# Kernel optimization log

Hardware: AMD Instinct MI355X
Metric: run time of the kernel (lower is better)

Reference implementation:

```python
import jax, jax.numpy as jnp
import numpy as np

D_MODEL = 512
NUM_HEADS = 8
D_K = D_MODEL // NUM_HEADS
EPS = 1e-8


def setup_inputs() -> dict:
    key = jax.random.key(0)
    ks = jax.random.split(key, 11)
    B, N = 2, 2048
    s = 1.0 / np.sqrt(D_MODEL)
    return {
        "query": jax.random.normal(ks[0], (B, N, D_MODEL), jnp.float32),
        "key": jax.random.normal(ks[1], (B, N, D_MODEL), jnp.float32),
        "value": jax.random.normal(ks[2], (B, N, D_MODEL), jnp.float32),
        "Wq": jax.random.uniform(ks[3], (D_MODEL, D_MODEL), jnp.float32, -s, s),
        "bq": jax.random.uniform(ks[4], (D_MODEL,), jnp.float32, -s, s),
        "Wk": jax.random.uniform(ks[5], (D_MODEL, D_MODEL), jnp.float32, -s, s),
        "bk": jax.random.uniform(ks[6], (D_MODEL,), jnp.float32, -s, s),
        "Wv": jax.random.uniform(ks[7], (D_MODEL, D_MODEL), jnp.float32, -s, s),
        "bv": jax.random.uniform(ks[8], (D_MODEL,), jnp.float32, -s, s),
        "Wo": jax.random.uniform(ks[9], (D_MODEL, D_MODEL), jnp.float32, -s, s),
        "bo": jax.random.uniform(ks[10], (D_MODEL,), jnp.float32, -s, s),
    }


def _heads(x, W, b, B):
    # torch Linear: x @ W.T + b ; then [B,N,H,dk] -> [B,H,N,dk]
    y = x @ W.T + b
    return y.reshape(B, -1, NUM_HEADS, D_K).transpose(0, 2, 1, 3)


def reference(query, key, value, Wq, bq, Wk, bk, Wv, bv, Wo, bo):
    B = query.shape[0]
    Q = _heads(query, Wq, bq, B)
    K = _heads(key, Wk, bk, B)
    V = _heads(value, Wv, bv, B)
    # elu(x) + 1 feature map
    Q = jax.nn.elu(Q) + 1.0
    K = jax.nn.elu(K) + 1.0
    # normalize Q over feature dim, K over sequence dim
    Qn = Q / (Q.sum(axis=-1, keepdims=True) + EPS)
    Kn = K / (K.sum(axis=-2, keepdims=True) + EPS)
    # explicit NxN context matrix (as in the original code)
    attention_weights = jnp.einsum("bhnd,bhmd->bhnm", Qn, Kn)  # [B,H,N,N]
    out = jnp.einsum("bhnm,bhmd->bhnd", attention_weights, V)   # [B,H,N,dk]
    out = out.transpose(0, 2, 1, 3).reshape(B, -1, D_MODEL)
    out = out @ Wo.T + bo
    return (out, attention_weights)
```

## Files before the change

### kernel.cpp

```cpp
#include <hip/hip_runtime.h>

#define B2    2
#define NSEQ  2048
#define DM    512
#define NH    8
#define DK    64
#define MROWS 4096
#define BH    (B2*NH)
#define BHSTR (NSEQ*DK)
#define EPSF  1e-8f
#define OUT0  (MROWS*DM)

typedef __attribute__((ext_vector_type(8))) short short8;
typedef __attribute__((ext_vector_type(4))) float f32x4;

union S8 { short8 v; short s[8]; };
union F4 { f32x4 v; float f[4]; };

__device__ float          g_Qp[MROWS*DM];
__device__ float          g_Kn[MROWS*DM];
__device__ float          g_Vh[MROWS*DM];
__device__ float          g_OH[MROWS*DM];
__device__ unsigned short g_Qbf[MROWS*DM];
__device__ unsigned short g_Kbf[MROWS*DM];
__device__ float          g_qinv[BH*NSEQ];
__device__ float          g_ksum[BH*DK];
__device__ float          g_KV[BH*DK*DK];

__device__ inline unsigned short f2bf(float x) {
    union { float f; unsigned u; } v; v.f = x;
    unsigned r = v.u + 0x7fffu + ((v.u >> 16) & 1u);
    return (unsigned short)(r >> 16);
}
__device__ inline float bf2f(unsigned short h) {
    union { unsigned u; float f; } v; v.u = ((unsigned)h) << 16; return v.f;
}
__device__ inline f32x4 mfma_bf16(short8 a, short8 b, f32x4 c) {
    return __builtin_amdgcn_mfma_f32_16x16x32_bf16(a, b, c, 0, 0, 0);
}

__global__ void zero_small() {
    int i = blockIdx.x * 256 + threadIdx.x;
    if (i < BH*DK*DK) g_KV[i] = 0.f;
    if (i < BH*DK)    g_ksum[i] = 0.f;
}

__global__ __launch_bounds__(256) void gemm_split(const float* __restrict__ A,
                                                  const float* __restrict__ W,
                                                  const float* __restrict__ bias,
                                                  float* __restrict__ dout, int mode) {
    __shared__ short Ah[128*56], Al[128*56], Bh_s[64*56], Bl_s[64*56];

    const float* Ap = (mode == 3) ? (const float*)g_OH : A;

    int t = threadIdx.x;
    int m0 = blockIdx.x * 128, n0 = blockIdx.y * 64;
    int lane = t & 63, w = t >> 6;
    int l15 = lane & 15, quad = lane >> 4;

    f32x4 acc[2][4];
    f32x4 z4 = {0.f, 0.f, 0.f, 0.f};
#pragma unroll
    for (int i = 0; i < 2; i++)
#pragma unroll
        for (int j = 0; j < 4; j++) acc[i][j] = z4;

    int ar = t >> 1, ac = (t & 1) * 16;
    int br = t >> 2, bc = (t & 3) * 8;

    for (int k0 = 0; k0 < 512; k0 += 32) {
        {
            const float* ag = Ap + (size_t)(m0 + ar) * 512 + k0 + ac;
            float xv[16];
            *(f32x4*)&xv[0]  = *(const f32x4*)(ag + 0);
            *(f32x4*)&xv[4]  = *(const f32x4*)(ag + 4);
            *(f32x4*)&xv[8]  = *(const f32x4*)(ag + 8);
            *(f32x4*)&xv[12] = *(const f32x4*)(ag + 12);
            S8 h0, h1, l0, l1;
#pragma unroll
            for (int i = 0; i < 8; i++) {
                float x = xv[i];
                unsigned short hb = f2bf(x);
                h0.s[i] = (short)hb;
                l0.s[i] = (short)f2bf(x - bf2f(hb));
            }
#pragma unroll
            for (int i = 0; i < 8; i++) {
                float x = xv[8 + i];
                unsigned short hb = f2bf(x);
                h1.s[i] = (short)hb;
                l1.s[i] = (short)f2bf(x - bf2f(hb));
            }
            *(short8*)&Ah[ar*56 + ac]     = h0.v;
            *(short8*)&Ah[ar*56 + ac + 8] = h1.v;
            *(short8*)&Al[ar*56 + ac]     = l0.v;
            *(short8*)&Al[ar*56 + ac + 8] = l1.v;
        }
        {
            const float* wg = W + (size_t)(n0 + br) * 512 + k0 + bc;
            float xv[8];
            *(f32x4*)&xv[0] = *(const f32x4*)(wg + 0);
            *(f32x4*)&xv[4] = *(const f32x4*)(wg + 4);
            S8 h0, l0;
#pragma unroll
            for (int i = 0; i < 8; i++) {
                float x = xv[i];
                unsigned short hb = f2bf(x);
                h0.s[i] = (short)hb;
                l0.s[i] = (short)f2bf(x - bf2f(hb));
            }
            *(short8*)&Bh_s[br*56 + bc] = h0.v;
            *(short8*)&Bl_s[br*56 + bc] = l0.v;
        }
        __syncthreads();

        int koff = quad * 8;
        short8 a_h[2], a_l[2], b_h[4], b_l[4];
#pragma unroll
        for (int i = 0; i < 2; i++) {
            int rr = (w*32 + i*16 + l15) * 56 + koff;
            a_h[i] = *(const short8*)&Ah[rr];
            a_l[i] = *(const short8*)&Al[rr];
        }
#pragma unroll
        for (int j = 0; j < 4; j++) {
            int rr = (j*16 + l15) * 56 + koff;
            b_h[j] = *(const short8*)&Bh_s[rr];
            b_l[j] = *(const short8*)&Bl_s[rr];
        }
#pragma unroll
        for (int i = 0; i < 2; i++)
#pragma unroll
            for (int j = 0; j < 4; j++) {
                acc[i][j] = mfma_bf16(a_h[i], b_h[j], acc[i][j]);
                acc[i][j] = mfma_bf16(a_h[i], b_l[j], acc[i][j]);
                acc[i][j] = mfma_bf16(a_l[i], b_h[j], acc[i][j]);
            }
        __syncthreads();
    }

#pragma unroll
    for (int j = 0; j < 4; j++) {
        int col = n0 + j*16 + l15;
        float bs = bias[col];
#pragma unroll
        for (int i = 0; i < 2; i++) {
            F4 v; v.v = acc[i][j];
#pragma unroll
            for (int r = 0; r < 4; r++) {
                int row = m0 + w*32 + i*16 + quad*4 + r;
                float val = v.f[r] + bs;
                if (mode == 3) {
                    dout[(size_t)row * 512 + col] = val;
                } else {
                    int bb = row >> 11, nn = row & 2047;
                    int hh = col >> 6,  dd = col & 63;
                    int dst = (bb*8 + hh) * BHSTR + nn*64 + dd;
                    if (mode == 2) {
                        g_Vh[dst] = val;
                    } else {
                        float e = (val > 0.f) ? (val + 1.f) : expf(val);
                        if (mode == 0) { g_Qp[dst] = e; g_Qbf[dst] = f2bf(e); }
                        else           { g_Kn[dst] = e; }
                    }
                }
            }
        }
    }
}

__global__ void qsum_kernel() {
    int t = threadIdx.x, w = t >> 6, lane = t & 63;
    int row = blockIdx.x * 4 + w;
    float v = g_Qp[(size_t)row * 64 + lane];
#pragma unroll
    for (int off = 32; off; off >>= 1) v += __shfl_down(v, off, 64);
    if (lane == 0) g_qinv[row] = 1.f / (v + EPSF);
}

__global__ void ksum_kernel() {
    int t = threadIdx.x;
    int bh = blockIdx.x >> 3, part = blockIdx.x & 7;
    int d = t & 63, sub = t >> 6;
    float s = 0.f;
    size_t base = (size_t)bh * BHSTR + (size_t)(part * 256) * 64 + d;
    for (int i = 0; i < 64; i++) s += g_Kn[base + (size_t)(sub + i*4) * 64];
    __shared__ float red[256];
    red[t] = s;
    __syncthreads();
    if (t < 64) {
        float tot = red[t] + red[t+64] + red[t+128] + red[t+192];
        atomicAdd(&g_ksum[bh*64 + d], tot);
    }
}

__global__ void knorm_kernel() {
    int gid = blockIdx.x * 256 + threadIdx.x;
    int i0 = gid * 4;
    int bh = i0 >> 17, d0 = i0 & 63;
    F4 v; v.v = *(const f32x4*)&g_Kn[i0];
    F4 o;
    unsigned short b[4];
#pragma unroll
    for (int j = 0; j < 4; j++) {
        float r = v.f[j] / (g_ksum[bh*64 + d0 + j] + EPSF);
        o.f[j] = r;
        b[j] = f2bf(r);
    }
    *(f32x4*)&g_Kn[i0] = o.v;
    unsigned long long packed = (unsigned long long)b[0] | ((unsigned long long)b[1] << 16)
                              | ((unsigned long long)b[2] << 32) | ((unsigned long long)b[3] << 48);
    *(unsigned long long*)&g_Kbf[i0] = packed;
}

__global__ __launch_bounds__(256) void attn_kernel(float* __restrict__ dout) {
    __shared__ short Qs[128*72], Ks[128*72];
    int bh = blockIdx.z;
    int m0 = blockIdx.x * 128, n0 = blockIdx.y * 128;
    int t = threadIdx.x, lane = t & 63, w = t >> 6;
    int l15 = lane & 15, quad = lane >> 4;

    int r = t >> 1, c0 = (t & 1) * 32;
    const short* qg = (const short*)g_Qbf + (size_t)bh * BHSTR + (size_t)(m0 + r) * 64 + c0;
    const short* kg = (const short*)g_Kbf + (size_t)bh * BHSTR + (size_t)(n0 + r) * 64 + c0;
#pragma unroll
    for (int i = 0; i < 4; i++) {
        *(short8*)&Qs[r*72 + c0 + 8*i] = *(const short8*)(qg + 8*i);
        *(short8*)&Ks[r*72 + c0 + 8*i] = *(const short8*)(kg + 8*i);
    }
    __syncthreads();

    int wm = (w >> 1) * 64, wn = (w & 1) * 64;
    f32x4 acc[4][4];
    f32x4 z4 = {0.f, 0.f, 0.f, 0.f};
#pragma unroll
    for (int i = 0; i < 4; i++)
#pragma unroll
        for (int j = 0; j < 4; j++) acc[i][j] = z4;

#pragma unroll
    for (int kk = 0; kk < 64; kk += 32) {
        short8 qa[4], kb[4];
#pragma unroll
        for (int i = 0; i < 4; i++) qa[i] = *(const short8*)&Qs[(wm + i*16 + l15)*72 + kk + quad*8];
#pragma unroll
        for (int j = 0; j < 4; j++) kb[j] = *(const short8*)&Ks[(wn + j*16 + l15)*72 + kk + quad*8];
#pragma unroll
        for (int i = 0; i < 4; i++)
#pragma unroll
            for (int j = 0; j < 4; j++) acc[i][j] = mfma_bf16(qa[i], kb[j], acc[i][j]);
    }

    float* outp = dout + OUT0 + (size_t)bh * NSEQ * NSEQ;
#pragma unroll
    for (int i = 0; i < 4; i++) {
#pragma unroll
        for (int r2 = 0; r2 < 4; r2++) {
            int row = m0 + wm + i*16 + quad*4 + r2;
            float qiv = g_qinv[bh*NSEQ + row];
#pragma unroll
            for (int j = 0; j < 4; j++) {
                int col = n0 + wn + j*16 + l15;
                F4 v; v.v = acc[i][j];
                outp[(size_t)row * NSEQ + col] = v.f[r2] * qiv;
            }
        }
    }
}

__global__ __launch_bounds__(256) void kv_kernel() {
    __shared__ float Ks2[64*64], Vs[64*64];
    int bh = blockIdx.x >> 4, part = blockIdx.x & 15;
    int t = threadIdx.x, d = t & 63, e0 = (t >> 6) * 16;
    float accv[16];
#pragma unroll
    for (int i = 0; i < 16; i++) accv[i] = 0.f;
    int sr = t >> 2, sc = (t & 3) * 16;
    for (int c = 0; c < 2; c++) {
        int nbase = part * 128 + c * 64;
        const float* kgp = g_Kn + (size_t)bh * BHSTR + (size_t)(nbase + sr) * 64 + sc;
        const float* vgp = g_Vh + (size_t)bh * BHSTR + (size_t)(nbase + sr) * 64 + sc;
#pragma unroll
        for (int i = 0; i < 4; i++) {
            *(f32x4*)&Ks2[sr*64 + sc + 4*i] = *(const f32x4*)(kgp + 4*i);
            *(f32x4*)&Vs[sr*64 + sc + 4*i]  = *(const f32x4*)(vgp + 4*i);
        }
        __syncthreads();
#pragma unroll 4
        for (int m = 0; m < 64; m++) {
            float v = Vs[m*64 + d];
            const f32x4* kr = (const f32x4*)&Ks2[m*64 + e0];
            F4 k0, k1, k2, k3;
            k0.v = kr[0]; k1.v = kr[1]; k2.v = kr[2]; k3.v = kr[3];
#pragma unroll
            for (int i = 0; i < 4; i++) accv[i]      += k0.f[i] * v;
#pragma unroll
            for (int i = 0; i < 4; i++) accv[4 + i]  += k1.f[i] * v;
#pragma unroll
            for (int i = 0; i < 4; i++) accv[8 + i]  += k2.f[i] * v;
#pragma unroll
            for (int i = 0; i < 4; i++) accv[12 + i] += k3.f[i] * v;
        }
        __syncthreads();
    }
#pragma unroll
    for (int i = 0; i < 16; i++)
        atomicAdd(&g_KV[bh*4096 + (e0 + i)*64 + d], accv[i]);
}

__global__ __launch_bounds__(256) void oh_kernel() {
    __shared__ float Qs2[128*64];
    __shared__ float KVs[64*64];
    int bh = blockIdx.y, r0 = blockIdx.x * 128;
    int t = threadIdx.x, d = t & 63, w = t >> 6;
    {
        int r = t >> 2, c = (t & 3) * 16;
        const float* s = g_KV + bh*4096 + r*64 + c;
#pragma unroll
        for (int i = 0; i < 4; i++) *(f32x4*)&KVs[r*64 + c + 4*i] = *(const f32x4*)(s + 4*i);
    }
    {
        int r = t >> 1, c = (t & 1) * 32;
        const float* s = g_Qp + (size_t)bh * BHSTR + (size_t)(r0 + r) * 64 + c;
#pragma unroll
        for (int i = 0; i < 8; i++) *(f32x4*)&Qs2[r*64 + c + 4*i] = *(const f32x4*)(s + 4*i);
    }
    __syncthreads();
    float kvc[64];
#pragma unroll
    for (int e = 0; e < 64; e++) kvc[e] = KVs[e*64 + d];
    int b = bh >> 3, h = bh & 7;
    for (int rr = 0; rr < 32; rr++) {
        int row = w * 32 + rr;
        const f32x4* qr = (const f32x4*)&Qs2[row*64];
        float a = 0.f;
#pragma unroll
        for (int e4 = 0; e4 < 16; e4++) {
            F4 q; q.v = qr[e4];
            a += q.f[0]*kvc[4*e4] + q.f[1]*kvc[4*e4+1] + q.f[2]*kvc[4*e4+2] + q.f[3]*kvc[4*e4+3];
        }
        int grow = r0 + row;
        float val = a * g_qinv[bh*NSEQ + grow];
        g_OH[((size_t)b*NSEQ + grow)*512 + h*64 + d] = val;
    }
}

extern "C" void kernel_launch(void* const* d_in, const int* in_sizes, int n_in,
                              void* d_out, int out_size, void* d_ws, size_t ws_size,
                              hipStream_t stream) {
    const float* q  = (const float*)d_in[0];
    const float* k  = (const float*)d_in[1];
    const float* v  = (const float*)d_in[2];
    const float* Wq = (const float*)d_in[3];
    const float* bq = (const float*)d_in[4];
    const float* Wk = (const float*)d_in[5];
    const float* bk = (const float*)d_in[6];
    const float* Wv = (const float*)d_in[7];
    const float* bv = (const float*)d_in[8];
    const float* Wo = (const float*)d_in[9];
    const float* bo = (const float*)d_in[10];
    float* out = (float*)d_out;

    zero_small<<<256, 256, 0, stream>>>();

    dim3 gproj(32, 8);
    gemm_split<<<gproj, 256, 0, stream>>>(q, Wq, bq, out, 0);
    gemm_split<<<gproj, 256, 0, stream>>>(k, Wk, bk, out, 1);
    gemm_split<<<gproj, 256, 0, stream>>>(v, Wv, bv, out, 2);

    qsum_kernel<<<8192, 256, 0, stream>>>();
    ksum_kernel<<<128, 256, 0, stream>>>();
    knorm_kernel<<<2048, 256, 0, stream>>>();

    attn_kernel<<<dim3(16, 16, BH), 256, 0, stream>>>(out);

    kv_kernel<<<256, 256, 0, stream>>>();
    oh_kernel<<<dim3(16, BH), 256, 0, stream>>>();

    gemm_split<<<gproj, 256, 0, stream>>>(nullptr, Wo, bo, out, 3);
}
```

Before: 471.5 us.

## Pre-split inputs to bf16, fuse normalization into GEMM epilogues, use direct-to-LDS loads

A new prep kernel converts inputs and weights to bf16 hi/lo pairs once, replacing the per-tile conversion inside the GEMMs. The GEMMs now load tiles with global_load_lds into XOR-swizzled shared memory. The K-sum, Q row sums and K normalization move into the GEMM epilogues, which removes the separate qsum, ksum and knorm kernels. V and the Wo input use a single bf16 term instead of the split, and intermediates are stored as bf16. This cuts conversion work, launches and memory traffic, but V and the output projection lose precision and K is rounded to bf16 before normalization.

Result: faster. 405.1 us (-14.1%).

```diff
diff --git a/kernel.cpp b/kernel.cpp
--- a/kernel.cpp
+++ b/kernel.cpp
@@ -1,62 +1,115 @@
 #include <hip/hip_runtime.h>
-
-#define B2    2
+#include <math.h>
+
 #define NSEQ  2048
 #define DM    512
 #define NH    8
 #define DK    64
 #define MROWS 4096
-#define BH    (B2*NH)
+#define BH    16
 #define BHSTR (NSEQ*DK)
+#define SLAB  (BH*BHSTR)
 #define EPSF  1e-8f
 #define OUT0  (MROWS*DM)
 
 typedef __attribute__((ext_vector_type(8))) short short8;
 typedef __attribute__((ext_vector_type(4))) float f32x4;
-
 union S8 { short8 v; short s[8]; };
 union F4 { f32x4 v; float f[4]; };
 
-__device__ float          g_Qp[MROWS*DM];
-__device__ float          g_Kn[MROWS*DM];
-__device__ float          g_Vh[MROWS*DM];
-__device__ float          g_OH[MROWS*DM];
-__device__ unsigned short g_Qbf[MROWS*DM];
-__device__ unsigned short g_Kbf[MROWS*DM];
+__device__ short g_qh[MROWS*DM], g_ql[MROWS*DM];
+__device__ short g_kh[MROWS*DM], g_kl[MROWS*DM];
+__device__ short g_vh[MROWS*DM];
+__device__ short g_wqh[DM*DM], g_wql[DM*DM];
+__device__ short g_wkh[DM*DM], g_wkl[DM*DM];
+__device__ short g_wvh[DM*DM], g_woh[DM*DM];
+__device__ unsigned short g_Qbf[SLAB];
+__device__ unsigned short g_Kbf[SLAB];
+__device__ float          g_Vf[SLAB];
+__device__ short          g_OHbf[MROWS*DM];
 __device__ float          g_qinv[BH*NSEQ];
 __device__ float          g_ksum[BH*DK];
 __device__ float          g_KV[BH*DK*DK];
 
-__device__ inline unsigned short f2bf(float x) {
+__device__ __forceinline__ unsigned short f2bf(float x) {
     union { float f; unsigned u; } v; v.f = x;
     unsigned r = v.u + 0x7fffu + ((v.u >> 16) & 1u);
     return (unsigned short)(r >> 16);
 }
-__device__ inline float bf2f(unsigned short h) {
+__device__ __forceinline__ float bf2f(unsigned short h) {
     union { unsigned u; float f; } v; v.u = ((unsigned)h) << 16; return v.f;
 }
-__device__ inline f32x4 mfma_bf16(short8 a, short8 b, f32x4 c) {
+__device__ __forceinline__ f32x4 mfma_bf16(short8 a, short8 b, f32x4 c) {
     return __builtin_amdgcn_mfma_f32_16x16x32_bf16(a, b, c, 0, 0, 0);
 }
-
-__global__ void zero_small() {
-    int i = blockIdx.x * 256 + threadIdx.x;
-    if (i < BH*DK*DK) g_KV[i] = 0.f;
-    if (i < BH*DK)    g_ksum[i] = 0.f;
-}
-
-__global__ __launch_bounds__(256) void gemm_split(const float* __restrict__ A,
-                                                  const float* __restrict__ W,
-                                                  const float* __restrict__ bias,
-                                                  float* __restrict__ dout, int mode) {
-    __shared__ short Ah[128*56], Al[128*56], Bh_s[64*56], Bl_s[64*56];
-
-    const float* Ap = (mode == 3) ? (const float*)g_OH : A;
-
-    int t = threadIdx.x;
+__device__ __forceinline__ float elu1(float x) {
+    return (x > 0.f) ? (x + 1.f) : __expf(x);
+}
+__device__ __forceinline__ void gl_lds16(const void* gsrc, void* ldst) {
+    __builtin_amdgcn_global_load_lds(
+        (__attribute__((address_space(1))) void*)(unsigned long long)(gsrc),
+        (__attribute__((address_space(3))) void*)(unsigned)(unsigned long long)(ldst),
+        16, 0, 0);
+}
+
+__global__ __launch_bounds__(256) void prep_kernel(const float* __restrict__ q, const float* __restrict__ k,
+                                                   const float* __restrict__ v, const float* __restrict__ wq,
+                                                   const float* __restrict__ wk, const float* __restrict__ wv,
+                                                   const float* __restrict__ wo) {
+    int b = blockIdx.x, t = threadIdx.x;
+    if (b < 33) {
+        int z = b * 2048 + t * 8;
+#pragma unroll
+        for (int i = 0; i < 8; i++) {
+            int zz = z + i;
+            if (zz < 65536) g_KV[zz] = 0.f;
+            else if (zz < 66560) g_ksum[zz - 65536] = 0.f;
+        }
+    }
+    const float* src; short* hi; short* lo; int off; int split;
+    if (b < 1024)      { src = q;  hi = g_qh;  lo = g_ql;  off = b * 2048;          split = 1; }
+    else if (b < 2048) { src = k;  hi = g_kh;  lo = g_kl;  off = (b-1024) * 2048;   split = 1; }
+    else if (b < 3072) { src = v;  hi = g_vh;  lo = g_vh;  off = (b-2048) * 2048;   split = 0; }
+    else if (b < 3200) { src = wq; hi = g_wqh; lo = g_wql; off = (b-3072) * 2048;   split = 1; }
+    else if (b < 3328) { src = wk; hi = g_wkh; lo = g_wkl; off = (b-3200) * 2048;   split = 1; }
+    else if (b < 3456) { src = wv; hi = g_wvh; lo = g_wvh; off = (b-3328) * 2048;   split = 0; }
+    else               { src = wo; hi = g_woh; lo = g_woh; off = (b-3456) * 2048;   split = 0; }
+    int idx = off + t * 8;
+    F4 a0, a1; a0.v = *(const f32x4*)(src + idx); a1.v = *(const f32x4*)(src + idx + 4);
+    S8 h, l;
+#pragma unroll
+    for (int i = 0; i < 4; i++) {
+        unsigned short hb = f2bf(a0.f[i]); h.s[i] = (short)hb;
+        l.s[i] = (short)f2bf(a0.f[i] - bf2f(hb));
+    }
+#pragma unroll
+    for (int i = 0; i < 4; i++) {
+        unsigned short hb = f2bf(a1.f[i]); h.s[4+i] = (short)hb;
+        l.s[4+i] = (short)f2bf(a1.f[i] - bf2f(hb));
+    }
+    *(short8*)(hi + idx) = h.v;
+    if (split) *(short8*)(lo + idx) = l.v;
+}
+
+template<int SPLIT>
+__global__ __launch_bounds__(256) void gemm_bf16(const float* __restrict__ bias,
+                                                 float* __restrict__ dout, int mode) {
+    __shared__ short sAh[128*64];
+    __shared__ short sBh[64*64];
+    __shared__ short sAl[SPLIT ? 128*64 : 8];
+    __shared__ short sBl[SPLIT ? 64*64 : 8];
+
+    const short *Ahi, *Alo = nullptr, *Bhi, *Blo = nullptr;
+    if (mode == 0)      { Ahi = g_qh;   Alo = g_ql;  Bhi = g_wqh; Blo = g_wql; }
+    else if (mode == 1) { Ahi = g_kh;   Alo = g_kl;  Bhi = g_wkh; Blo = g_wkl; }
+    else if (mode == 2) { Ahi = g_vh;   Bhi = g_wvh; }
+    else                { Ahi = g_OHbf; Bhi = g_woh; }
+
+    int t = threadIdx.x, lane = t & 63, w = t >> 6;
+    int l15 = lane & 15, quad = lane >> 4;
     int m0 = blockIdx.x * 128, n0 = blockIdx.y * 64;
-    int lane = t & 63, w = t >> 6;
-    int l15 = lane & 15, quad = lane >> 4;
+    int r_in = lane >> 3, gq = lane & 7;
+    int scol = (gq ^ r_in) << 3;
 
     f32x4 acc[2][4];
     f32x4 z4 = {0.f, 0.f, 0.f, 0.f};
@@ -65,168 +118,162 @@
 #pragma unroll
         for (int j = 0; j < 4; j++) acc[i][j] = z4;
 
-    int ar = t >> 1, ac = (t & 1) * 16;
-    int br = t >> 2, bc = (t & 3) * 8;
-
-    for (int k0 = 0; k0 < 512; k0 += 32) {
-        {
-            const float* ag = Ap + (size_t)(m0 + ar) * 512 + k0 + ac;
-            float xv[16];
-            *(f32x4*)&xv[0]  = *(const f32x4*)(ag + 0);
-            *(f32x4*)&xv[4]  = *(const f32x4*)(ag + 4);
-            *(f32x4*)&xv[8]  = *(const f32x4*)(ag + 8);
-            *(f32x4*)&xv[12] = *(const f32x4*)(ag + 12);
-            S8 h0, h1, l0, l1;
-#pragma unroll
-            for (int i = 0; i < 8; i++) {
-                float x = xv[i];
-                unsigned short hb = f2bf(x);
-                h0.s[i] = (short)hb;
-                l0.s[i] = (short)f2bf(x - bf2f(hb));
-            }
-#pragma unroll
-            for (int i = 0; i < 8; i++) {
-                float x = xv[8 + i];
-                unsigned short hb = f2bf(x);
-                h1.s[i] = (short)hb;
-                l1.s[i] = (short)f2bf(x - bf2f(hb));
-            }
-            *(short8*)&Ah[ar*56 + ac]     = h0.v;
-            *(short8*)&Ah[ar*56 + ac + 8] = h1.v;
-            *(short8*)&Al[ar*56 + ac]     = l0.v;
-            *(short8*)&Al[ar*56 + ac + 8] = l1.v;
-        }
-        {
-            const float* wg = W + (size_t)(n0 + br) * 512 + k0 + bc;
-            float xv[8];
-            *(f32x4*)&xv[0] = *(const f32x4*)(wg + 0);
-            *(f32x4*)&xv[4] = *(const f32x4*)(wg + 4);
-            S8 h0, l0;
-#pragma unroll
-            for (int i = 0; i < 8; i++) {
-                float x = xv[i];
-                unsigned short hb = f2bf(x);
-                h0.s[i] = (short)hb;
-                l0.s[i] = (short)f2bf(x - bf2f(hb));
-            }
-            *(short8*)&Bh_s[br*56 + bc] = h0.v;
-            *(short8*)&Bl_s[br*56 + bc] = l0.v;
+    for (int k0 = 0; k0 < 512; k0 += 64) {
+#pragma unroll
+        for (int ii = 0; ii < 4; ii++) {
+            int i = w * 4 + ii;
+            size_t so = (size_t)(m0 + i*8 + r_in) * 512 + k0 + scol;
+            gl_lds16(Ahi + so, &sAh[i * 512]);
+            if (SPLIT) gl_lds16(Alo + so, &sAl[i * 512]);
+        }
+#pragma unroll
+        for (int ii = 0; ii < 2; ii++) {
+            int i = w * 2 + ii;
+            size_t so = (size_t)(n0 + i*8 + r_in) * 512 + k0 + scol;
+            gl_lds16(Bhi + so, &sBh[i * 512]);
+            if (SPLIT) gl_lds16(Blo + so, &sBl[i * 512]);
         }
         __syncthreads();
 
-        int koff = quad * 8;
-        short8 a_h[2], a_l[2], b_h[4], b_l[4];
-#pragma unroll
-        for (int i = 0; i < 2; i++) {
-            int rr = (w*32 + i*16 + l15) * 56 + koff;
-            a_h[i] = *(const short8*)&Ah[rr];
-            a_l[i] = *(const short8*)&Al[rr];
-        }
-#pragma unroll
-        for (int j = 0; j < 4; j++) {
-            int rr = (j*16 + l15) * 56 + koff;
-            b_h[j] = *(const short8*)&Bh_s[rr];
-            b_l[j] = *(const short8*)&Bl_s[rr];
-        }
-#pragma unroll
-        for (int i = 0; i < 2; i++)
+#pragma unroll
+        for (int ks = 0; ks < 2; ks++) {
+            int kg = ks * 4 + quad;
+            int sw = (kg ^ (l15 & 7)) << 3;
+            short8 ah[2], al[2], bh[4], bl[4];
+#pragma unroll
+            for (int i = 0; i < 2; i++) {
+                int ad = (w*32 + i*16 + l15) * 64 + sw;
+                ah[i] = *(const short8*)&sAh[ad];
+                if (SPLIT) al[i] = *(const short8*)&sAl[ad];
+            }
 #pragma unroll
             for (int j = 0; j < 4; j++) {
-                acc[i][j] = mfma_bf16(a_h[i], b_h[j], acc[i][j]);
-                acc[i][j] = mfma_bf16(a_h[i], b_l[j], acc[i][j]);
-                acc[i][j] = mfma_bf16(a_l[i], b_h[j], acc[i][j]);
-            }
-        __syncthreads();
-    }
-
-#pragma unroll
-    for (int j = 0; j < 4; j++) {
-        int col = n0 + j*16 + l15;
-        float bs = bias[col];
-#pragma unroll
-        for (int i = 0; i < 2; i++) {
-            F4 v; v.v = acc[i][j];
-#pragma unroll
-            for (int r = 0; r < 4; r++) {
-                int row = m0 + w*32 + i*16 + quad*4 + r;
-                float val = v.f[r] + bs;
-                if (mode == 3) {
-                    dout[(size_t)row * 512 + col] = val;
-                } else {
-                    int bb = row >> 11, nn = row & 2047;
-                    int hh = col >> 6,  dd = col & 63;
-                    int dst = (bb*8 + hh) * BHSTR + nn*64 + dd;
-                    if (mode == 2) {
-                        g_Vh[dst] = val;
-                    } else {
-                        float e = (val > 0.f) ? (val + 1.f) : expf(val);
-                        if (mode == 0) { g_Qp[dst] = e; g_Qbf[dst] = f2bf(e); }
-                        else           { g_Kn[dst] = e; }
+                int ad = (j*16 + l15) * 64 + sw;
+                bh[j] = *(const short8*)&sBh[ad];
+                if (SPLIT) bl[j] = *(const short8*)&sBl[ad];
+            }
+#pragma unroll
+            for (int i = 0; i < 2; i++)
+#pragma unroll
+                for (int j = 0; j < 4; j++) {
+                    acc[i][j] = mfma_bf16(ah[i], bh[j], acc[i][j]);
+                    if (SPLIT) {
+                        acc[i][j] = mfma_bf16(ah[i], bl[j], acc[i][j]);
+                        acc[i][j] = mfma_bf16(al[i], bh[j], acc[i][j]);
                     }
                 }
-            }
-        }
-    }
-}
-
-__global__ void qsum_kernel() {
-    int t = threadIdx.x, w = t >> 6, lane = t & 63;
-    int row = blockIdx.x * 4 + w;
-    float v = g_Qp[(size_t)row * 64 + lane];
-#pragma unroll
-    for (int off = 32; off; off >>= 1) v += __shfl_down(v, off, 64);
-    if (lane == 0) g_qinv[row] = 1.f / (v + EPSF);
-}
-
-__global__ void ksum_kernel() {
-    int t = threadIdx.x;
-    int bh = blockIdx.x >> 3, part = blockIdx.x & 7;
-    int d = t & 63, sub = t >> 6;
-    float s = 0.f;
-    size_t base = (size_t)bh * BHSTR + (size_t)(part * 256) * 64 + d;
-    for (int i = 0; i < 64; i++) s += g_Kn[base + (size_t)(sub + i*4) * 64];
-    __shared__ float red[256];
-    red[t] = s;
-    __syncthreads();
-    if (t < 64) {
-        float tot = red[t] + red[t+64] + red[t+128] + red[t+192];
-        atomicAdd(&g_ksum[bh*64 + d], tot);
-    }
-}
-
-__global__ void knorm_kernel() {
-    int gid = blockIdx.x * 256 + threadIdx.x;
-    int i0 = gid * 4;
-    int bh = i0 >> 17, d0 = i0 & 63;
-    F4 v; v.v = *(const f32x4*)&g_Kn[i0];
-    F4 o;
-    unsigned short b[4];
-#pragma unroll
-    for (int j = 0; j < 4; j++) {
-        float r = v.f[j] / (g_ksum[bh*64 + d0 + j] + EPSF);
-        o.f[j] = r;
-        b[j] = f2bf(r);
-    }
-    *(f32x4*)&g_Kn[i0] = o.v;
-    unsigned long long packed = (unsigned long long)b[0] | ((unsigned long long)b[1] << 16)
-                              | ((unsigned long long)b[2] << 32) | ((unsigned long long)b[3] << 48);
-    *(unsigned long long*)&g_Kbf[i0] = packed;
+        }
+        __syncthreads();
+    }
+
+    int head = blockIdx.y;
+    int bh16 = ((m0 >> 11) << 3) + head;
+    if (mode == 3) {
+#pragma unroll
+        for (int j = 0; j < 4; j++) {
+            int col = n0 + j*16 + l15;
+            float bsv = bias[col];
+#pragma unroll
+            for (int i = 0; i < 2; i++) {
+                F4 v; v.v = acc[i][j];
+#pragma unroll
+                for (int r = 0; r < 4; r++) {
+                    int row = m0 + w*32 + i*16 + quad*4 + r;
+                    dout[(size_t)row * 512 + col] = v.f[r] + bsv;
+                }
+            }
+        }
+    } else if (mode == 2) {
+#pragma unroll
+        for (int j = 0; j < 4; j++) {
+            int col = n0 + j*16 + l15;
+            float bsv = bias[col];
+            int dd = col & 63;
+#pragma unroll
+            for (int i = 0; i < 2; i++) {
+                F4 v; v.v = acc[i][j];
+#pragma unroll
+                for (int r = 0; r < 4; r++) {
+                    int nn = (m0 + w*32 + i*16 + quad*4 + r) & 2047;
+                    g_Vf[(size_t)bh16 * BHSTR + nn*64 + dd] = v.f[r] + bsv;
+                }
+            }
+        }
+    } else {
+        float e[2][4][4];
+#pragma unroll
+        for (int j = 0; j < 4; j++) {
+            float bsv = bias[n0 + j*16 + l15];
+#pragma unroll
+            for (int i = 0; i < 2; i++) {
+                F4 v; v.v = acc[i][j];
+#pragma unroll
+                for (int r = 0; r < 4; r++) e[i][j][r] = elu1(v.f[r] + bsv);
+            }
+        }
+        if (mode == 0) {
+            float rks[4];
+#pragma unroll
+            for (int j = 0; j < 4; j++)
+                rks[j] = 1.f / (g_ksum[bh16*64 + j*16 + l15] + EPSF);
+#pragma unroll
+            for (int i = 0; i < 2; i++) {
+#pragma unroll
+                for (int r = 0; r < 4; r++) {
+                    float s = e[i][0][r] + e[i][1][r] + e[i][2][r] + e[i][3][r];
+                    s += __shfl_xor(s, 1); s += __shfl_xor(s, 2);
+                    s += __shfl_xor(s, 4); s += __shfl_xor(s, 8);
+                    if (l15 == 0) {
+                        int nn = (m0 + w*32 + i*16 + quad*4 + r) & 2047;
+                        g_qinv[bh16*NSEQ + nn] = 1.f / (s + EPSF);
+                    }
+                }
+#pragma unroll
+                for (int j = 0; j < 4; j++) {
+                    int dd = j*16 + l15;
+#pragma unroll
+                    for (int r = 0; r < 4; r++) {
+                        int nn = (m0 + w*32 + i*16 + quad*4 + r) & 2047;
+                        g_Qbf[(size_t)bh16 * BHSTR + nn*64 + dd] = f2bf(e[i][j][r] * rks[j]);
+                    }
+                }
+            }
+        } else {
+#pragma unroll
+            for (int j = 0; j < 4; j++) {
+                int dd = j*16 + l15;
+                float s = 0.f;
+#pragma unroll
+                for (int i = 0; i < 2; i++)
+#pragma unroll
+                    for (int r = 0; r < 4; r++) {
+                        int nn = (m0 + w*32 + i*16 + quad*4 + r) & 2047;
+                        g_Kbf[(size_t)bh16 * BHSTR + nn*64 + dd] = f2bf(e[i][j][r]);
+                        s += e[i][j][r];
+                    }
+                s += __shfl_xor(s, 16); s += __shfl_xor(s, 32);
+                if (lane < 16) atomicAdd(&g_ksum[bh16*64 + dd], s);
+            }
+        }
+    }
 }
 
 __global__ __launch_bounds__(256) void attn_kernel(float* __restrict__ dout) {
-    __shared__ short Qs[128*72], Ks[128*72];
+    __shared__ short Qs[128*64], Ks[128*64];
     int bh = blockIdx.z;
     int m0 = blockIdx.x * 128, n0 = blockIdx.y * 128;
     int t = threadIdx.x, lane = t & 63, w = t >> 6;
     int l15 = lane & 15, quad = lane >> 4;
-
-    int r = t >> 1, c0 = (t & 1) * 32;
-    const short* qg = (const short*)g_Qbf + (size_t)bh * BHSTR + (size_t)(m0 + r) * 64 + c0;
-    const short* kg = (const short*)g_Kbf + (size_t)bh * BHSTR + (size_t)(n0 + r) * 64 + c0;
-#pragma unroll
-    for (int i = 0; i < 4; i++) {
-        *(short8*)&Qs[r*72 + c0 + 8*i] = *(const short8*)(qg + 8*i);
-        *(short8*)&Ks[r*72 + c0 + 8*i] = *(const short8*)(kg + 8*i);
+    int r_in = lane >> 3, gq = lane & 7;
+    int scol = (gq ^ r_in) << 3;
+
+    const short* qb = (const short*)g_Qbf + (size_t)bh * BHSTR;
+    const short* kb = (const short*)g_Kbf + (size_t)bh * BHSTR;
+#pragma unroll
+    for (int ii = 0; ii < 4; ii++) {
+        int i = w * 4 + ii;
+        gl_lds16(qb + (size_t)(m0 + i*8 + r_in) * 64 + scol, &Qs[i * 512]);
+        gl_lds16(kb + (size_t)(n0 + i*8 + r_in) * 64 + scol, &Ks[i * 512]);
     }
     __syncthreads();
 
@@ -239,16 +286,18 @@
         for (int j = 0; j < 4; j++) acc[i][j] = z4;
 
 #pragma unroll
-    for (int kk = 0; kk < 64; kk += 32) {
-        short8 qa[4], kb[4];
-#pragma unroll
-        for (int i = 0; i < 4; i++) qa[i] = *(const short8*)&Qs[(wm + i*16 + l15)*72 + kk + quad*8];
-#pragma unroll
-        for (int j = 0; j < 4; j++) kb[j] = *(const short8*)&Ks[(wn + j*16 + l15)*72 + kk + quad*8];
+    for (int ks = 0; ks < 2; ks++) {
+        int kg = ks * 4 + quad;
+        int sw = (kg ^ (l15 & 7)) << 3;
+        short8 qa[4], kbf[4];
+#pragma unroll
+        for (int i = 0; i < 4; i++) qa[i]  = *(const short8*)&Qs[(wm + i*16 + l15) * 64 + sw];
+#pragma unroll
+        for (int j = 0; j < 4; j++) kbf[j] = *(const short8*)&Ks[(wn + j*16 + l15) * 64 + sw];
 #pragma unroll
         for (int i = 0; i < 4; i++)
 #pragma unroll
-            for (int j = 0; j < 4; j++) acc[i][j] = mfma_bf16(qa[i], kb[j], acc[i][j]);
+            for (int j = 0; j < 4; j++) acc[i][j] = mfma_bf16(qa[i], kbf[j], acc[i][j]);
     }
 
     float* outp = dout + OUT0 + (size_t)bh * NSEQ * NSEQ;
@@ -260,9 +309,8 @@
             float qiv = g_qinv[bh*NSEQ + row];
 #pragma unroll
             for (int j = 0; j < 4; j++) {
-                int col = n0 + wn + j*16 + l15;
                 F4 v; v.v = acc[i][j];
-                outp[(size_t)row * NSEQ + col] = v.f[r2] * qiv;
+                outp[(size_t)row * NSEQ + (n0 + wn + j*16 + l15)] = v.f[r2] * qiv;
             }
         }
     }
@@ -278,28 +326,33 @@
     int sr = t >> 2, sc = (t & 3) * 16;
     for (int c = 0; c < 2; c++) {
         int nbase = part * 128 + c * 64;
-        const float* kgp = g_Kn + (size_t)bh * BHSTR + (size_t)(nbase + sr) * 64 + sc;
-        const float* vgp = g_Vh + (size_t)bh * BHSTR + (size_t)(nbase + sr) * 64 + sc;
-#pragma unroll
-        for (int i = 0; i < 4; i++) {
-            *(f32x4*)&Ks2[sr*64 + sc + 4*i] = *(const f32x4*)(kgp + 4*i);
-            *(f32x4*)&Vs[sr*64 + sc + 4*i]  = *(const f32x4*)(vgp + 4*i);
-        }
+        const unsigned short* kgp = g_Qbf, *dummy = kgp; (void)dummy;
+        kgp = g_Kbf + (size_t)bh * BHSTR + (size_t)(nbase + sr) * 64 + sc;
+        const float* vgp = g_Vf + (size_t)bh * BHSTR + (size_t)(nbase + sr) * 64 + sc;
+        S8 k0, k1;
+        k0.v = *(const short8*)(kgp);
+        k1.v = *(const short8*)(kgp + 8);
+#pragma unroll
+        for (int i = 0; i < 8; i++) Ks2[sr*64 + sc + i]     = bf2f((unsigned short)k0.s[i]);
+#pragma unroll
+        for (int i = 0; i < 8; i++) Ks2[sr*64 + sc + 8 + i] = bf2f((unsigned short)k1.s[i]);
+#pragma unroll
+        for (int i = 0; i < 4; i++) *(f32x4*)&Vs[sr*64 + sc + 4*i] = *(const f32x4*)(vgp + 4*i);
         __syncthreads();
 #pragma unroll 4
         for (int m = 0; m < 64; m++) {
             float v = Vs[m*64 + d];
             const f32x4* kr = (const f32x4*)&Ks2[m*64 + e0];
-            F4 k0, k1, k2, k3;
-            k0.v = kr[0]; k1.v = kr[1]; k2.v = kr[2]; k3.v = kr[3];
-#pragma unroll
-            for (int i = 0; i < 4; i++) accv[i]      += k0.f[i] * v;
-#pragma unroll
-            for (int i = 0; i < 4; i++) accv[4 + i]  += k1.f[i] * v;
-#pragma unroll
-            for (int i = 0; i < 4; i++) accv[8 + i]  += k2.f[i] * v;
-#pragma unroll
-            for (int i = 0; i < 4; i++) accv[12 + i] += k3.f[i] * v;
+            F4 q0, q1, q2, q3;
+            q0.v = kr[0]; q1.v = kr[1]; q2.v = kr[2]; q3.v = kr[3];
+#pragma unroll
+            for (int i = 0; i < 4; i++) accv[i]      += q0.f[i] * v;
+#pragma unroll
+            for (int i = 0; i < 4; i++) accv[4 + i]  += q1.f[i] * v;
+#pragma unroll
+            for (int i = 0; i < 4; i++) accv[8 + i]  += q2.f[i] * v;
+#pragma unroll
+            for (int i = 0; i < 4; i++) accv[12 + i] += q3.f[i] * v;
         }
         __syncthreads();
     }
@@ -321,9 +374,13 @@
     }
     {
         int r = t >> 1, c = (t & 1) * 32;
-        const float* s = g_Qp + (size_t)bh * BHSTR + (size_t)(r0 + r) * 64 + c;
-#pragma unroll
-        for (int i = 0; i < 8; i++) *(f32x4*)&Qs2[r*64 + c + 4*i] = *(const f32x4*)(s + 4*i);
+        const unsigned short* s = g_Qbf + (size_t)bh * BHSTR + (size_t)(r0 + r) * 64 + c;
+#pragma unroll
+        for (int i = 0; i < 4; i++) {
+            S8 x; x.v = *(const short8*)(s + 8*i);
+#pragma unroll
+            for (int j = 0; j < 8; j++) Qs2[r*64 + c + 8*i + j] = bf2f((unsigned short)x.s[j]);
+        }
     }
     __syncthreads();
     float kvc[64];
@@ -341,7 +398,7 @@
         }
         int grow = r0 + row;
         float val = a * g_qinv[bh*NSEQ + grow];
-        g_OH[((size_t)b*NSEQ + grow)*512 + h*64 + d] = val;
+        g_OHbf[((size_t)b*NSEQ + grow)*512 + h*64 + d] = (short)f2bf(val);
     }
 }
 
@@ -361,21 +418,17 @@
     const float* bo = (const float*)d_in[10];
     float* out = (float*)d_out;
 
-    zero_small<<<256, 256, 0, stream>>>();
+    prep_kernel<<<3584, 256, 0, stream>>>(q, k, v, Wq, Wk, Wv, Wo);
 
     dim3 gproj(32, 8);
-    gemm_split<<<gproj, 256, 0, stream>>>(q, Wq, bq, out, 0);
-    gemm_split<<<gproj, 256, 0, stream>>>(k, Wk, bk, out, 1);
-    gemm_split<<<gproj, 256, 0, stream>>>(v, Wv, bv, out, 2);
-
-    qsum_kernel<<<8192, 256, 0, stream>>>();
-    ksum_kernel<<<128, 256, 0, stream>>>();
-    knorm_kernel<<<2048, 256, 0, stream>>>();
+    gemm_bf16<1><<<gproj, 256, 0, stream>>>(bk, nullptr, 1);
+    gemm_bf16<1><<<gproj, 256, 0, stream>>>(bq, nullptr, 0);
+    gemm_bf16<0><<<gproj, 256, 0, stream>>>(bv, nullptr, 2);
 
     attn_kernel<<<dim3(16, 16, BH), 256, 0, stream>>>(out);
 
     kv_kernel<<<256, 256, 0, stream>>>();
     oh_kernel<<<dim3(16, BH), 256, 0, stream>>>();
 
-    gemm_split<<<gproj, 256, 0, stream>>>(nullptr, Wo, bo, out, 3);
-}
+    gemm_bf16<0><<<gproj, 256, 0, stream>>>(bo, out, 3);
+}
```
